# Kernel tuning notes

Hardware: AMD Instinct MI355X
Metric: run time of the kernel (lower is better)

The kernel has to match this reference:

```python
import jax, jax.numpy as jnp
from jax import lax
import numpy as np

B, N, F_IN = 8, 8192, 64
NPOINT, K = 2048, 16
C0 = F_IN + 3  # use_xyz concat
EPS = 1e-5


def setup_inputs() -> dict:
    key = jax.random.key(0)
    ks = jax.random.split(key, 8)
    xyz = jax.random.normal(ks[0], (B, 3, N), dtype=jnp.float32)
    points = jax.random.normal(ks[1], (B, F_IN, N), dtype=jnp.float32)
    def conv_params(k, cout, cin):
        W = jax.random.normal(k, (cout, cin), dtype=jnp.float32) * (1.0 / np.sqrt(cin))
        return W, jnp.zeros((cout,), jnp.float32)
    W1, b1 = conv_params(ks[2], 64, C0)
    W2, b2 = conv_params(ks[3], 64, 64)
    W3, b3 = conv_params(ks[4], 128, 64)
    g1 = jnp.ones((64,), jnp.float32); be1 = jnp.zeros((64,), jnp.float32)
    g2 = jnp.ones((64,), jnp.float32); be2 = jnp.zeros((64,), jnp.float32)
    return dict(xyz=xyz, points=points, W1=W1, b1=b1, g1=g1, be1=be1,
                W2=W2, b2=b2, g2=g2, be2=be2, W3=W3, b3=b3)


def _fps(xyz_bn3, npoint):
    # furthest point sampling; starts at index 0 (as PointNet++ CUDA op)
    b, n, _ = xyz_bn3.shape
    init_idx = jnp.zeros((b,), jnp.int32)
    dist0 = jnp.full((b, n), 1e10, xyz_bn3.dtype)

    def body(carry, _):
        dist, last = carry
        p = jnp.take_along_axis(xyz_bn3, last[:, None, None], axis=1)  # (b,1,3)
        d = jnp.sum((xyz_bn3 - p) ** 2, axis=-1)                       # (b,n)
        dist = jnp.minimum(dist, d)
        nxt = jnp.argmax(dist, axis=-1).astype(jnp.int32)
        return (dist, nxt), nxt

    (_, _), rest = lax.scan(body, (dist0, init_idx), None, length=npoint - 1)
    return jnp.concatenate([init_idx[None], rest], axis=0).T  # (b, npoint)


def _gather_feat(feat, idx):
    # feat: (B,C,N), idx: (B,...) -> (B,C,...)
    return jax.vmap(lambda f, i: f[:, i])(feat, idx)


def _conv_bn_relu(x, W, b, g, be):
    # 1x1 Conv2d + BatchNorm2d(training batch stats) + ReLU
    y = jnp.einsum('oi,bipk->bopk', W, x) + b[None, :, None, None]
    mean = y.mean(axis=(0, 2, 3))
    var = y.var(axis=(0, 2, 3))
    y = (y - mean[None, :, None, None]) * lax.rsqrt(var + EPS)[None, :, None, None]
    y = y * g[None, :, None, None] + be[None, :, None, None]
    return jax.nn.relu(y)


def reference(xyz, points, W1, b1, g1, be1, W2, b2, g2, be2, W3, b3):
    # --- sample_and_group_knn ---
    xyz_t = jnp.transpose(xyz, (0, 2, 1))             # (B,N,3)
    fps_idx = _fps(xyz_t, NPOINT)                      # (B,npoint)
    new_xyz = _gather_feat(xyz, fps_idx)               # (B,3,npoint)
    q = jnp.transpose(new_xyz, (0, 2, 1))              # (B,npoint,3)
    # squared distances (B,npoint,N)
    sq = (jnp.sum(q ** 2, -1)[:, :, None]
          + jnp.sum(xyz_t ** 2, -1)[:, None, :]
          - 2.0 * jnp.einsum('bqc,bnc->bqn', q, xyz_t))
    _, idx = lax.top_k(-sq, K)                         # (B,npoint,K) nearest
    grouped_xyz = _gather_feat(xyz, idx)               # (B,3,npoint,K)
    grouped_xyz = grouped_xyz - new_xyz[:, :, :, None]
    grouped_pts = _gather_feat(points, idx)            # (B,f,npoint,K)
    new_points = jnp.concatenate([grouped_xyz, grouped_pts], axis=1)  # (B,67,npoint,K)
    # --- shared MLP (1x1 convs) + max-pool over neighbors ---
    h = _conv_bn_relu(new_points, W1, b1, g1, be1)
    h = _conv_bn_relu(h, W2, b2, g2, be2)
    h = jnp.einsum('oi,bipk->bopk', W3, h) + b3[None, :, None, None]  # no bn/act
    new_feat = jnp.max(h, axis=3)                      # (B,128,npoint)
    return new_xyz, new_feat
```

## Files before the change

### kernel.cpp

```cpp
#include <hip/hip_runtime.h>
#pragma clang fp contract(off)

#define BB 8
#define NN 8192
#define NP 2048
#define KNbr 16
#define FIN 64
#define NPOS (BB*NP*KNbr)
#define NCONS 248
#define AG __HIP_MEMORY_SCOPE_AGENT

typedef float f32x2 __attribute__((ext_vector_type(2)));
typedef unsigned long long u64;

__device__ __forceinline__ float sq3(float x, float y, float z) {
  return __fadd_rn(__fadd_rn(__fmul_rn(x,x), __fmul_rn(y,y)), __fmul_rn(z,z));
}

__device__ __forceinline__ int wave_imax(int x) {
  x = max(x, __builtin_amdgcn_update_dpp(0, x, 0x111, 0xf, 0xf, false));
  x = max(x, __builtin_amdgcn_update_dpp(0, x, 0x112, 0xf, 0xf, false));
  x = max(x, __builtin_amdgcn_update_dpp(0, x, 0x114, 0xf, 0xf, false));
  x = max(x, __builtin_amdgcn_update_dpp(0, x, 0x118, 0xf, 0xf, false));
  x = max(x, __builtin_amdgcn_update_dpp(0, x, 0x142, 0xa, 0xf, false));
  x = max(x, __builtin_amdgcn_update_dpp(0, x, 0x143, 0xc, 0xf, false));
  return __builtin_amdgcn_readlane(x, 63);
}
__device__ __forceinline__ unsigned wave_umin(unsigned x) {
  x = min(x, (unsigned)__builtin_amdgcn_update_dpp(-1, (int)x, 0x111, 0xf, 0xf, false));
  x = min(x, (unsigned)__builtin_amdgcn_update_dpp(-1, (int)x, 0x112, 0xf, 0xf, false));
  x = min(x, (unsigned)__builtin_amdgcn_update_dpp(-1, (int)x, 0x114, 0xf, 0xf, false));
  x = min(x, (unsigned)__builtin_amdgcn_update_dpp(-1, (int)x, 0x118, 0xf, 0xf, false));
  x = min(x, (unsigned)__builtin_amdgcn_update_dpp(-1, (int)x, 0x142, 0xa, 0xf, false));
  x = min(x, (unsigned)__builtin_amdgcn_update_dpp(-1, (int)x, 0x143, 0xc, 0xf, false));
  return (unsigned)__builtin_amdgcn_readlane((int)x, 63);
}

__global__ __launch_bounds__(256,1) void k_front2(const float* __restrict__ xyz,
                                                  const float* __restrict__ pts,
                                                  const float* __restrict__ W1,
                                                  const float* __restrict__ b1,
                                                  float4* __restrict__ xyzw,
                                                  float* __restrict__ qwf,
                                                  float* __restrict__ pre,
                                                  float* __restrict__ stats,
                                                  int* __restrict__ prog,
                                                  int* __restrict__ pflag,
                                                  float* __restrict__ ybuf,
                                                  float* __restrict__ newxyz) {
  __shared__ float tx[NN], ty[NN], tz[NN];
  __shared__ float4 res[NP];
  __shared__ u64 skey[2][4];
  int blk = blockIdx.x, tid = threadIdx.x;
  int lane = tid & 63, wave = tid >> 6;

  if (blk >= 8) {
    for (int g = (blk-8)*256 + tid; g < BB*NN; g += NCONS*256) {
      int b = g >> 13, n = g & (NN-1);
      const float* p = xyz + (size_t)b*3*NN;
      float x = p[n], y = p[NN+n], z = p[2*NN+n];
      xyzw[g] = make_float4(x, y, z, sq3(x,y,z));
      const float* P = pts + (size_t)b*FIN*NN + n;
      float pv[64];
      #pragma unroll
      for (int i=0;i<64;++i) pv[i] = P[(size_t)i*NN];
      float4* outp = (float4*)(pre + (size_t)g*64);
      for (int og=0; og<16; ++og) {
        float acc[4];
        #pragma unroll
        for (int oo=0;oo<4;++oo) {
          int o = og*4+oo;
          float s = b1[o];
          #pragma unroll
          for (int i=0;i<64;++i) s = fmaf(W1[o*67+3+i], pv[i], s);
          acc[oo] = s;
        }
        outp[og] = make_float4(acc[0],acc[1],acc[2],acc[3]);
      }
    }
    if (blk == 8) stats[tid] = 0.f;
    __syncthreads();
    if (tid == 0) {
      __threadfence();
      __hip_atomic_store(&pflag[blk-8], 1, __ATOMIC_RELEASE, AG);
    }
    bool ok = false;
    while (!ok) {
      int v = 1;
      for (int i = lane; i < NCONS; i += 64)
        v &= (__hip_atomic_load(&pflag[i], __ATOMIC_RELAXED, AG) == 1);
      ok = (bool)__all(v);
      if (!ok) __builtin_amdgcn_s_sleep(32);
    }
    __threadfence();

    int slot = (blk-8)*4 + wave;
    float W1a = W1[lane*67+0], W1b = W1[lane*67+1], W1c = W1[lane*67+2];
    float sum = 0.f, ss = 0.f;
    for (int qi = slot; qi < BB*NP; qi += NCONS*4) {
      int t = qi >> 3, b = qi & 7;
      while (__hip_atomic_load(&prog[b*32], __ATOMIC_RELAXED, AG) <= t)
        __builtin_amdgcn_s_sleep(16);
      const float* qp = qwf + ((size_t)(b*NP + t))*4;
      float qx  = __hip_atomic_load(qp+0, __ATOMIC_RELAXED, AG);
      float qy  = __hip_atomic_load(qp+1, __ATOMIC_RELAXED, AG);
      float qz  = __hip_atomic_load(qp+2, __ATOMIC_RELAXED, AG);
      float qw4 = __hip_atomic_load(qp+3, __ATOMIC_RELAXED, AG);
      const float4* base = xyzw + (size_t)b*NN;
      float ld = 3.0e38f; int li = 0x7fffffff;
      float taud = 3.0e38f; int taui = 0x7fffffff;
      for (int c = 0; c < 128; ++c) {
        int idx = c*64 + lane;
        float4 P = base[idx];
        float dot = __fadd_rn(__fadd_rn(__fmul_rn(P.x,qx), __fmul_rn(P.y,qy)), __fmul_rn(P.z,qz));
        float dd  = __fsub_rn(__fadd_rn(qw4, P.w), __fmul_rn(2.0f, dot));
        bool better = (dd < taud) || (dd == taud && idx < taui);
        u64 mask = __ballot(better);
        while (mask) {
          int src = __ffsll(mask) - 1;
          mask &= mask - 1;
          float bd = __shfl(dd, src, 64);
          int   bi = __shfl(idx, src, 64);
          bool before = (ld < bd) || (ld == bd && li < bi);
          float sd = __shfl_up(ld, 1, 64);
          int   si = __shfl_up(li, 1, 64);
          int   bp = __shfl_up((int)before, 1, 64);
          bool take_new = !before && (lane == 0 || bp);
          float nd = before ? ld : (take_new ? bd : sd);
          int   ni = before ? li : (take_new ? bi : si);
          if (lane < 16) { ld = nd; li = ni; }
          taud = __shfl(ld, 15, 64);
          taui = __shfl(li, 15, 64);
        }
      }
      const float* preb = pre + (size_t)b*NN*64;
      float* yb = ybuf + ((size_t)(b*NP + t))*16*64;
      for (int l=0;l<16;++l) {
        int n = __shfl(li, l, 64);
        float4 P = base[n];
        float dx=__fsub_rn(P.x,qx), dy=__fsub_rn(P.y,qy), dz=__fsub_rn(P.z,qz);
        float v = fmaf(W1a, dx, fmaf(W1b, dy, fmaf(W1c, dz, preb[(size_t)n*64 + lane])));
        yb[l*64 + lane] = v;
        sum += v; ss = fmaf(v, v, ss);
      }
    }
    atomicAdd(&stats[lane], sum);
    atomicAdd(&stats[64+lane], ss);
    return;
  }

  int b = blk;
  const float* pxyz = xyz + (size_t)b*3*NN;
  f32x2 px[16], py[16], pz[16], d2[16];
  #pragma unroll
  for (int j=0;j<16;++j) {
    int i = j*512 + 2*tid;
    float2 xv = *(const float2*)(pxyz + i);
    float2 yv = *(const float2*)(pxyz + NN + i);
    float2 zv = *(const float2*)(pxyz + 2*NN + i);
    tx[i] = xv.x; tx[i+1] = xv.y;
    ty[i] = yv.x; ty[i+1] = yv.y;
    tz[i] = zv.x; tz[i+1] = zv.y;
    px[j] = f32x2{xv.x, xv.y};
    py[j] = f32x2{yv.x, yv.y};
    pz[j] = f32x2{zv.x, zv.y};
    d2[j] = f32x2{1e10f, 1e10f};
  }
  float cx = pxyz[0], cy = pxyz[NN], cz = pxyz[2*NN];
  if (tid==0) {
    res[0] = make_float4(cx, cy, cz, 0.f);
    __hip_atomic_store(qwf + (size_t)(b*NP)*4 + 0, cx, __ATOMIC_RELAXED, AG);
    __hip_atomic_store(qwf + (size_t)(b*NP)*4 + 1, cy, __ATOMIC_RELAXED, AG);
    __hip_atomic_store(qwf + (size_t)(b*NP)*4 + 2, cz, __ATOMIC_RELAXED, AG);
    __hip_atomic_store(qwf + (size_t)(b*NP)*4 + 3, sq3(cx,cy,cz), __ATOMIC_RELAXED, AG);
    __hip_atomic_store(&prog[b*32], 1, __ATOMIC_RELEASE, AG);
  }
  int w = tid>>6;
  __syncthreads();
  for (int t=1;t<NP;++t) {
    f32x2 cx2 = {cx,cx}, cy2 = {cy,cy}, cz2 = {cz,cz};
    #pragma unroll
    for (int j=0;j<16;++j) {
      f32x2 dx = px[j]-cx2, dy = py[j]-cy2, dz = pz[j]-cz2;
      f32x2 dd = (dx*dx + dy*dy) + dz*dz;
#if __has_builtin(__builtin_elementwise_min)
      d2[j] = __builtin_elementwise_min(d2[j], dd);
#else
      d2[j].x = fminf(d2[j].x, dd.x);
      d2[j].y = fminf(d2[j].y, dd.y);
#endif
    }
    float tv[16]; int tk[16];
    #pragma unroll
    for (int j=0;j<16;++j) {
      bool r = d2[j].y > d2[j].x;
      tv[j] = r ? d2[j].y : d2[j].x;
      tk[j] = r ? 2*j+1 : 2*j;
    }
    #pragma unroll
    for (int j=0;j<8;++j) { bool r = tv[j+8] > tv[j]; if (r){tv[j]=tv[j+8]; tk[j]=tk[j+8];} }
    #pragma unroll
    for (int j=0;j<4;++j) { bool r = tv[j+4] > tv[j]; if (r){tv[j]=tv[j+4]; tk[j]=tk[j+4];} }
    #pragma unroll
    for (int j=0;j<2;++j) { bool r = tv[j+2] > tv[j]; if (r){tv[j]=tv[j+2]; tk[j]=tk[j+2];} }
    bool rr = tv[1] > tv[0];
    float lmax = rr ? tv[1] : tv[0];
    int   k    = rr ? tk[1] : tk[0];
    unsigned gidx = (unsigned)((k>>1)*512 + 2*tid + (k&1));
    int mb = wave_imax(__float_as_int(lmax));
    unsigned cand = (__float_as_int(lmax) == mb) ? gidx : 0xFFFFFFFFu;
    unsigned wwin = wave_umin(cand);
    int buf = t & 1;
    if ((tid & 63) == 0)
      skey[buf][w] = ((u64)(unsigned)mb << 32) | (u64)(0xFFFFFFFFu - wwin);
    __syncthreads();
    if ((t & 63) == 0) {
      int e = t - 64 + (tid >> 2), comp = tid & 3;
      float4 r = res[e];
      float v = (comp==0) ? r.x : (comp==1) ? r.y : (comp==2) ? r.z : sq3(r.x,r.y,r.z);
      __hip_atomic_store(qwf + ((size_t)(b*NP + e))*4 + comp, v, __ATOMIC_RELAXED, AG);
    } else if ((t & 63) == 1 && t > 64 && tid == 0) {
      __hip_atomic_store(&prog[b*32], t-1, __ATOMIC_RELEASE, AG);
    }
    u64 mk = skey[buf][0];
    if (skey[buf][1] > mk) mk = skey[buf][1];
    if (skey[buf][2] > mk) mk = skey[buf][2];
    if (skey[buf][3] > mk) mk = skey[buf][3];
    unsigned widx = 0xFFFFFFFFu - (unsigned)(mk & 0xFFFFFFFFull);
    cx = tx[widx]; cy = ty[widx]; cz = tz[widx];
    if (tid == (t & 255))
      res[t] = make_float4(cx, cy, cz, 0.f);
  }
  __syncthreads();
  float* outx = newxyz + (size_t)b*3*NP;
  #pragma unroll
  for (int s=0;s<8;++s) {
    int i = s*256 + tid;
    float4 r = res[i];
    *(float4*)(qwf + ((size_t)(b*NP + i))*4) = make_float4(r.x, r.y, r.z, sq3(r.x,r.y,r.z));
    outx[i] = r.x; outx[NP + i] = r.y; outx[2*NP + i] = r.z;
  }
  __syncthreads();
  if (tid == 0) {
    __threadfence();
    __hip_atomic_store(&prog[b*32], NP, __ATOMIC_RELEASE, AG);
  }
}

__device__ __forceinline__ float dot64(const float4* x, const float* W, float init) {
  float a0 = init, a1 = 0.f, a2 = 0.f, a3 = 0.f;
  #pragma unroll
  for (int j=0;j<16;++j) {
    float4 v = x[j];
    a0 = fmaf(v.x, W[4*j],   a0);
    a1 = fmaf(v.y, W[4*j+1], a1);
    a2 = fmaf(v.z, W[4*j+2], a2);
    a3 = fmaf(v.w, W[4*j+3], a3);
  }
  return (a0+a1)+(a2+a3);
}

__global__ __launch_bounds__(256) void k_conv2f(float* __restrict__ y,
                                                const float* __restrict__ W2,
                                                const float* __restrict__ b2,
                                                const float* __restrict__ st1,
                                                const float* __restrict__ g1,
                                                const float* __restrict__ be1,
                                                float* __restrict__ st2) {
  __shared__ __align__(16) float4 xs[1024];
  __shared__ __align__(16) float sS[64], sT[64];
  __shared__ float r1[4][64], r2[4][64];
  int tid = threadIdx.x, lane = tid & 63, wave = tid >> 6;
  if (tid < 64) {
    float mean = st1[tid] * (1.0f/NPOS);
    float var  = st1[64+tid] * (1.0f/NPOS) - mean*mean;
    float istd = 1.0f / sqrtf(var + 1e-5f);
    float s = g1[tid]*istd;
    sS[tid] = s;
    sT[tid] = be1[tid] - mean*s;
  }
  float W[64];
  #pragma unroll
  for (int j=0;j<16;++j) {
    float4 t = *(const float4*)(W2 + (size_t)lane*64 + j*4);
    W[4*j]=t.x; W[4*j+1]=t.y; W[4*j+2]=t.z; W[4*j+3]=t.w;
  }
  float bb = b2[lane];
  __syncthreads();
  size_t tbase = (size_t)blockIdx.x * 1024;
  float4* Y4 = (float4*)y;
  #pragma unroll
  for (int i=0;i<4;++i) {
    int idx = i*256 + tid;
    float4 v = Y4[tbase + idx];
    int c0 = (idx & 15)*4;
    float4 s4 = *(const float4*)(sS + c0);
    float4 t4 = *(const float4*)(sT + c0);
    v.x = fmaxf(0.f, fmaf(v.x, s4.x, t4.x));
    v.y = fmaxf(0.f, fmaf(v.y, s4.y, t4.y));
    v.z = fmaxf(0.f, fmaf(v.z, s4.z, t4.z));
    v.w = fmaxf(0.f, fmaf(v.w, s4.w, t4.w));
    xs[idx] = v;
  }
  __syncthreads();
  float sum = 0.f, ss = 0.f;
  size_t pos0 = (size_t)blockIdx.x*64 + wave*16;
  #pragma unroll 1
  for (int p=0;p<16;++p) {
    float acc = dot64(&xs[(wave*16+p)*16], W, bb);
    y[(pos0+p)*64 + lane] = acc;
    sum += acc; ss = fmaf(acc, acc, ss);
  }
  r1[wave][lane] = sum; r2[wave][lane] = ss;
  __syncthreads();
  if (tid < 64) {
    float t1 = r1[0][tid]+r1[1][tid]+r1[2][tid]+r1[3][tid];
    float t2 = r2[0][tid]+r2[1][tid]+r2[2][tid]+r2[3][tid];
    atomicAdd(&st2[tid], t1);
    atomicAdd(&st2[64+tid], t2);
  }
}

__global__ __launch_bounds__(256) void k_c3f(const float* __restrict__ y,
                                             const float* __restrict__ W3,
                                             const float* __restrict__ b3,
                                             const float* __restrict__ st2,
                                             const float* __restrict__ g2,
                                             const float* __restrict__ be2,
                                             float* __restrict__ feat) {
  __shared__ __align__(16) float4 xs[1024];
  __shared__ __align__(16) float sS[64], sT[64];
  int tid = threadIdx.x, lane = tid & 63, wave = tid >> 6;
  int h = wave & 1, qpair = wave >> 1;
  if (tid < 64) {
    float mean = st2[tid] * (1.0f/NPOS);
    float var  = st2[64+tid] * (1.0f/NPOS) - mean*mean;
    float istd = 1.0f / sqrtf(var + 1e-5f);
    float s = g2[tid]*istd;
    sS[tid] = s;
    sT[tid] = be2[tid] - mean*s;
  }
  int O = h*64 + lane;
  float W[64];
  #pragma unroll
  for (int j=0;j<16;++j) {
    float4 t = *(const float4*)(W3 + (size_t)O*64 + j*4);
    W[4*j]=t.x; W[4*j+1]=t.y; W[4*j+2]=t.z; W[4*j+3]=t.w;
  }
  float bb = b3[O];
  __syncthreads();
  size_t tbase = (size_t)blockIdx.x * 1024;
  const float4* Y4 = (const float4*)y;
  #pragma unroll
  for (int i=0;i<4;++i) {
    int idx = i*256 + tid;
    float4 v = Y4[tbase + idx];
    int c0 = (idx & 15)*4;
    float4 s4 = *(const float4*)(sS + c0);
    float4 t4 = *(const float4*)(sT + c0);
    v.x = fmaxf(0.f, fmaf(v.x, s4.x, t4.x));
    v.y = fmaxf(0.f, fmaf(v.y, s4.y, t4.y));
    v.z = fmaxf(0.f, fmaf(v.z, s4.z, t4.z));
    v.w = fmaxf(0.f, fmaf(v.w, s4.w, t4.w));
    xs[idx] = v;
  }
  __syncthreads();
  float mq[2];
  #pragma unroll 1
  for (int q=0;q<2;++q) {
    float m = -3.0e38f;
    #pragma unroll 1
    for (int k=0;k<16;++k) {
      int p = (qpair*2 + q)*16 + k;
      m = fmaxf(m, dot64(&xs[p*16], W, bb));
    }
    mq[q] = m;
  }
  int gq0 = blockIdx.x*4 + qpair*2;
  int b = gq0 >> 11, qq = gq0 & (NP-1);
  float* fp = feat + ((size_t)(b*128 + O))*NP + qq;
  fp[0] = mq[0];
  fp[1] = mq[1];
}

extern "C" void kernel_launch(void* const* d_in, const int* in_sizes, int n_in,
                              void* d_out, int out_size, void* d_ws, size_t ws_size,
                              hipStream_t stream) {
  const float* xyz = (const float*)d_in[0];
  const float* pts = (const float*)d_in[1];
  const float* W1  = (const float*)d_in[2];
  const float* b1  = (const float*)d_in[3];
  const float* g1  = (const float*)d_in[4];
  const float* be1 = (const float*)d_in[5];
  const float* W2  = (const float*)d_in[6];
  const float* b2  = (const float*)d_in[7];
  const float* g2  = (const float*)d_in[8];
  const float* be2 = (const float*)d_in[9];
  const float* W3  = (const float*)d_in[10];
  const float* b3  = (const float*)d_in[11];
  float* out = (float*)d_out;
  float* ws  = (float*)d_ws;

  float4* xyzw  = (float4*)ws;
  float*  qwf   = ws + 262144;
  float*  pre   = ws + 1654784;
  float*  ybuf  = ws + 5849088;
  float*  stats = ws + 22626304;
  int*    prog  = (int*)(ws + 22626560);
  int*    pflag = (int*)(ws + 22626816);

  k_front2<<<256, 256, 0, stream>>>(xyz, pts, W1, b1, xyzw, qwf, pre, stats,
                                    prog, pflag, ybuf, out);
  k_conv2f<<<4096, 256, 0, stream>>>(ybuf, W2, b2, stats, g1, be1, stats + 128);
  k_c3f   <<<4096, 256, 0, stream>>>(ybuf, W3, b3, stats + 128, g2, be2, out + 49152);
}
```

Baseline: 2.333 ms.

## Fuse FPS wave argmax into one key reduction; double-tile conv kernels with prefetch

```diff
diff --git a/kernel.cpp b/kernel.cpp
--- a/kernel.cpp
+++ b/kernel.cpp
@@ -17,23 +17,18 @@
   return __fadd_rn(__fadd_rn(__fmul_rn(x,x), __fmul_rn(y,y)), __fmul_rn(z,z));
 }
 
-__device__ __forceinline__ int wave_imax(int x) {
-  x = max(x, __builtin_amdgcn_update_dpp(0, x, 0x111, 0xf, 0xf, false));
-  x = max(x, __builtin_amdgcn_update_dpp(0, x, 0x112, 0xf, 0xf, false));
-  x = max(x, __builtin_amdgcn_update_dpp(0, x, 0x114, 0xf, 0xf, false));
-  x = max(x, __builtin_amdgcn_update_dpp(0, x, 0x118, 0xf, 0xf, false));
-  x = max(x, __builtin_amdgcn_update_dpp(0, x, 0x142, 0xa, 0xf, false));
-  x = max(x, __builtin_amdgcn_update_dpp(0, x, 0x143, 0xc, 0xf, false));
-  return __builtin_amdgcn_readlane(x, 63);
-}
-__device__ __forceinline__ unsigned wave_umin(unsigned x) {
-  x = min(x, (unsigned)__builtin_amdgcn_update_dpp(-1, (int)x, 0x111, 0xf, 0xf, false));
-  x = min(x, (unsigned)__builtin_amdgcn_update_dpp(-1, (int)x, 0x112, 0xf, 0xf, false));
-  x = min(x, (unsigned)__builtin_amdgcn_update_dpp(-1, (int)x, 0x114, 0xf, 0xf, false));
-  x = min(x, (unsigned)__builtin_amdgcn_update_dpp(-1, (int)x, 0x118, 0xf, 0xf, false));
-  x = min(x, (unsigned)__builtin_amdgcn_update_dpp(-1, (int)x, 0x142, 0xa, 0xf, false));
-  x = min(x, (unsigned)__builtin_amdgcn_update_dpp(-1, (int)x, 0x143, 0xc, 0xf, false));
-  return (unsigned)__builtin_amdgcn_readlane((int)x, 63);
+__device__ __forceinline__ u64 wave_kmax(unsigned hi, unsigned lo) {
+#define KSTEP(ctrl, rmask) { \
+    unsigned oh = (unsigned)__builtin_amdgcn_update_dpp(0, (int)hi, ctrl, rmask, 0xf, false); \
+    unsigned ol = (unsigned)__builtin_amdgcn_update_dpp(0, (int)lo, ctrl, rmask, 0xf, false); \
+    bool g = (oh > hi) || (oh == hi && ol > lo); \
+    hi = g ? oh : hi; lo = g ? ol : lo; }
+  KSTEP(0x111,0xf) KSTEP(0x112,0xf) KSTEP(0x114,0xf) KSTEP(0x118,0xf)
+  KSTEP(0x142,0xa) KSTEP(0x143,0xc)
+#undef KSTEP
+  unsigned mh = (unsigned)__builtin_amdgcn_readlane((int)hi, 63);
+  unsigned ml = (unsigned)__builtin_amdgcn_readlane((int)lo, 63);
+  return ((u64)mh << 32) | (u64)ml;
 }
 
 __global__ __launch_bounds__(256,1) void k_front2(const float* __restrict__ xyz,
@@ -51,6 +46,7 @@
   __shared__ float tx[NN], ty[NN], tz[NN];
   __shared__ float4 res[NP];
   __shared__ u64 skey[2][4];
+  __shared__ float4 scen[2][4];
   int blk = blockIdx.x, tid = threadIdx.x;
   int lane = tid & 63, wave = tid >> 6;
 
@@ -207,12 +203,15 @@
     float lmax = rr ? tv[1] : tv[0];
     int   k    = rr ? tk[1] : tk[0];
     unsigned gidx = (unsigned)((k>>1)*512 + 2*tid + (k&1));
-    int mb = wave_imax(__float_as_int(lmax));
-    unsigned cand = (__float_as_int(lmax) == mb) ? gidx : 0xFFFFFFFFu;
-    unsigned wwin = wave_umin(cand);
+    unsigned khi = (unsigned)__float_as_int(lmax);
+    unsigned klo = 0xFFFFFFFFu - gidx;
+    u64 wk = wave_kmax(khi, klo);
     int buf = t & 1;
-    if ((tid & 63) == 0)
-      skey[buf][w] = ((u64)(unsigned)mb << 32) | (u64)(0xFFFFFFFFu - wwin);
+    if (khi == (unsigned)(wk >> 32) && klo == (unsigned)wk) {
+      float wx = tx[gidx], wy = ty[gidx], wz = tz[gidx];
+      skey[buf][w] = wk;
+      scen[buf][w] = make_float4(wx, wy, wz, 0.f);
+    }
     __syncthreads();
     if ((t & 63) == 0) {
       int e = t - 64 + (tid >> 2), comp = tid & 3;
@@ -222,12 +221,12 @@
     } else if ((t & 63) == 1 && t > 64 && tid == 0) {
       __hip_atomic_store(&prog[b*32], t-1, __ATOMIC_RELEASE, AG);
     }
-    u64 mk = skey[buf][0];
-    if (skey[buf][1] > mk) mk = skey[buf][1];
-    if (skey[buf][2] > mk) mk = skey[buf][2];
-    if (skey[buf][3] > mk) mk = skey[buf][3];
-    unsigned widx = 0xFFFFFFFFu - (unsigned)(mk & 0xFFFFFFFFull);
-    cx = tx[widx]; cy = ty[widx]; cz = tz[widx];
+    u64 k0 = skey[buf][0], k1 = skey[buf][1], k2 = skey[buf][2], k3 = skey[buf][3];
+    float4 c0 = scen[buf][0], c1 = scen[buf][1], c2 = scen[buf][2], c3 = scen[buf][3];
+    bool gA = k1 > k0; u64 kA = gA ? k1 : k0; float4 cA = gA ? c1 : c0;
+    bool gB = k3 > k2; u64 kB = gB ? k3 : k2; float4 cB = gB ? c3 : c2;
+    float4 cw = (kB > kA) ? cB : cA;
+    cx = cw.x; cy = cw.y; cz = cw.z;
     if (tid == (t & 255))
       res[t] = make_float4(cx, cy, cz, 0.f);
   }
@@ -286,30 +285,41 @@
     W[4*j]=t.x; W[4*j+1]=t.y; W[4*j+2]=t.z; W[4*j+3]=t.w;
   }
   float bb = b2[lane];
-  __syncthreads();
-  size_t tbase = (size_t)blockIdx.x * 1024;
   float4* Y4 = (float4*)y;
-  #pragma unroll
-  for (int i=0;i<4;++i) {
-    int idx = i*256 + tid;
-    float4 v = Y4[tbase + idx];
-    int c0 = (idx & 15)*4;
-    float4 s4 = *(const float4*)(sS + c0);
-    float4 t4 = *(const float4*)(sT + c0);
-    v.x = fmaxf(0.f, fmaf(v.x, s4.x, t4.x));
-    v.y = fmaxf(0.f, fmaf(v.y, s4.y, t4.y));
-    v.z = fmaxf(0.f, fmaf(v.z, s4.z, t4.z));
-    v.w = fmaxf(0.f, fmaf(v.w, s4.w, t4.w));
-    xs[idx] = v;
-  }
+  size_t base0 = (size_t)blockIdx.x * 2048;
+  float4 r[4];
+  #pragma unroll
+  for (int i=0;i<4;++i) r[i] = Y4[base0 + i*256 + tid];
   __syncthreads();
   float sum = 0.f, ss = 0.f;
-  size_t pos0 = (size_t)blockIdx.x*64 + wave*16;
   #pragma unroll 1
-  for (int p=0;p<16;++p) {
-    float acc = dot64(&xs[(wave*16+p)*16], W, bb);
-    y[(pos0+p)*64 + lane] = acc;
-    sum += acc; ss = fmaf(acc, acc, ss);
+  for (int tI=0; tI<2; ++tI) {
+    #pragma unroll
+    for (int i=0;i<4;++i) {
+      int idx = i*256 + tid;
+      float4 v = r[i];
+      int c0 = (idx & 15)*4;
+      float4 s4 = *(const float4*)(sS + c0);
+      float4 t4 = *(const float4*)(sT + c0);
+      v.x = fmaxf(0.f, fmaf(v.x, s4.x, t4.x));
+      v.y = fmaxf(0.f, fmaf(v.y, s4.y, t4.y));
+      v.z = fmaxf(0.f, fmaf(v.z, s4.z, t4.z));
+      v.w = fmaxf(0.f, fmaf(v.w, s4.w, t4.w));
+      xs[idx] = v;
+    }
+    __syncthreads();
+    if (tI == 0) {
+      #pragma unroll
+      for (int i=0;i<4;++i) r[i] = Y4[base0 + 1024 + i*256 + tid];
+    }
+    size_t pos0 = (size_t)blockIdx.x*128 + tI*64 + wave*16;
+    #pragma unroll 1
+    for (int p=0;p<16;++p) {
+      float acc = dot64(&xs[(wave*16+p)*16], W, bb);
+      y[(pos0+p)*64 + lane] = acc;
+      sum += acc; ss = fmaf(acc, acc, ss);
+    }
+    __syncthreads();
   }
   r1[wave][lane] = sum; r2[wave][lane] = ss;
   __syncthreads();
@@ -348,39 +358,50 @@
     W[4*j]=t.x; W[4*j+1]=t.y; W[4*j+2]=t.z; W[4*j+3]=t.w;
   }
   float bb = b3[O];
-  __syncthreads();
-  size_t tbase = (size_t)blockIdx.x * 1024;
   const float4* Y4 = (const float4*)y;
-  #pragma unroll
-  for (int i=0;i<4;++i) {
-    int idx = i*256 + tid;
-    float4 v = Y4[tbase + idx];
-    int c0 = (idx & 15)*4;
-    float4 s4 = *(const float4*)(sS + c0);
-    float4 t4 = *(const float4*)(sT + c0);
-    v.x = fmaxf(0.f, fmaf(v.x, s4.x, t4.x));
-    v.y = fmaxf(0.f, fmaf(v.y, s4.y, t4.y));
-    v.z = fmaxf(0.f, fmaf(v.z, s4.z, t4.z));
-    v.w = fmaxf(0.f, fmaf(v.w, s4.w, t4.w));
-    xs[idx] = v;
-  }
-  __syncthreads();
-  float mq[2];
+  size_t base0 = (size_t)blockIdx.x * 2048;
+  float4 r[4];
+  #pragma unroll
+  for (int i=0;i<4;++i) r[i] = Y4[base0 + i*256 + tid];
+  __syncthreads();
   #pragma unroll 1
-  for (int q=0;q<2;++q) {
-    float m = -3.0e38f;
+  for (int tI=0; tI<2; ++tI) {
+    #pragma unroll
+    for (int i=0;i<4;++i) {
+      int idx = i*256 + tid;
+      float4 v = r[i];
+      int c0 = (idx & 15)*4;
+      float4 s4 = *(const float4*)(sS + c0);
+      float4 t4 = *(const float4*)(sT + c0);
+      v.x = fmaxf(0.f, fmaf(v.x, s4.x, t4.x));
+      v.y = fmaxf(0.f, fmaf(v.y, s4.y, t4.y));
+      v.z = fmaxf(0.f, fmaf(v.z, s4.z, t4.z));
+      v.w = fmaxf(0.f, fmaf(v.w, s4.w, t4.w));
+      xs[idx] = v;
+    }
+    __syncthreads();
+    if (tI == 0) {
+      #pragma unroll
+      for (int i=0;i<4;++i) r[i] = Y4[base0 + 1024 + i*256 + tid];
+    }
+    float mq[2];
     #pragma unroll 1
-    for (int k=0;k<16;++k) {
-      int p = (qpair*2 + q)*16 + k;
-      m = fmaxf(m, dot64(&xs[p*16], W, bb));
-    }
-    mq[q] = m;
-  }
-  int gq0 = blockIdx.x*4 + qpair*2;
-  int b = gq0 >> 11, qq = gq0 & (NP-1);
-  float* fp = feat + ((size_t)(b*128 + O))*NP + qq;
-  fp[0] = mq[0];
-  fp[1] = mq[1];
+    for (int q=0;q<2;++q) {
+      float m = -3.0e38f;
+      #pragma unroll 1
+      for (int k=0;k<16;++k) {
+        int p = (qpair*2 + q)*16 + k;
+        m = fmaxf(m, dot64(&xs[p*16], W, bb));
+      }
+      mq[q] = m;
+    }
+    int gq0 = blockIdx.x*8 + tI*4 + qpair*2;
+    int b = gq0 >> 11, qq = gq0 & (NP-1);
+    float* fp = feat + ((size_t)(b*128 + O))*NP + qq;
+    fp[0] = mq[0];
+    fp[1] = mq[1];
+    __syncthreads();
+  }
 }
 
 extern "C" void kernel_launch(void* const* d_in, const int* in_sizes, int n_in,
@@ -411,6 +432,6 @@
 
   k_front2<<<256, 256, 0, stream>>>(xyz, pts, W1, b1, xyzw, qwf, pre, stats,
                                     prog, pflag, ybuf, out);
-  k_conv2f<<<4096, 256, 0, stream>>>(ybuf, W2, b2, stats, g1, be1, stats + 128);
-  k_c3f   <<<4096, 256, 0, stream>>>(ybuf, W3, b3, stats + 128, g2, be2, out + 49152);
-}
+  k_conv2f<<<2048, 256, 0, stream>>>(ybuf, W2, b2, stats, g1, be1, stats + 128);
+  k_c3f   <<<2048, 256, 0, stream>>>(ybuf, W3, b3, stats + 128, g2, be2, out + 49152);
+}
```

Result: slower. 2.800 ms (+20.0%).
